# Kernel optimization log

Hardware: AMD Instinct MI355X
Metric: run time of the kernel (lower is better)

Reference implementation:

```python
import jax, jax.numpy as jnp
import numpy as np

EPS = 1e-6

def _rms(x, w):
    # RMSNorm over last dim with learned scale w
    var = jnp.mean(x * x, axis=-1, keepdims=True)
    return x * jax.lax.rsqrt(var + EPS) * w

def _split_heads(x, h):
    b, l, hd = x.shape
    return x.reshape(b, l, h, hd // h).transpose(0, 2, 1, 3)  # b h l d

def setup_inputs() -> dict:
    key = jax.random.key(0)
    ks = jax.random.split(key, 12)
    D = 2048          # hidden_size == ip_hidden_states_dim
    H = 16            # n_heads
    Dh = 128          # head_dim
    T = 1280          # timesteps_emb_dim
    B, L, Lip = 2, 2048, 512
    s = 0.02
    return {
        "ip_hidden_states": jax.random.normal(ks[0], (B, Lip, D), jnp.float32),
        "img_query": jax.random.normal(ks[1], (B, L, D), jnp.float32),
        "img_key": jax.random.normal(ks[2], (B, L, D), jnp.float32),
        "img_value": jax.random.normal(ks[3], (B, L, D), jnp.float32),
        "t_emb": jax.random.normal(ks[4], (B, T), jnp.float32),
        "W_ada": jax.random.normal(ks[5], (2 * D, T), jnp.float32) * s,
        "b_ada": jax.random.normal(ks[6], (2 * D,), jnp.float32) * s,
        "W_k_ip": jax.random.normal(ks[7], (D, D), jnp.float32) * s,
        "W_v_ip": jax.random.normal(ks[8], (D, D), jnp.float32) * s,
        "w_q": jnp.ones((Dh,), jnp.float32),
        "w_k": jnp.ones((Dh,), jnp.float32),
        "w_ipk": jnp.ones((Dh,), jnp.float32),
        "n_heads": H,
    }

def reference(ip_hidden_states, img_query, img_key, img_value, t_emb,
              W_ada, b_ada, W_k_ip, W_v_ip, w_q, w_k, w_ipk, n_heads):
    D = img_query.shape[-1]
    # AdaLayerNorm (mode='normal'): silu -> linear -> shift/scale, LN(no affine)
    emb = jax.nn.silu(t_emb) @ W_ada.T + b_ada          # [B, 2D]
    shift, scale = emb[:, :D], emb[:, D:]
    x = ip_hidden_states
    mu = jnp.mean(x, axis=-1, keepdims=True)
    var = jnp.mean((x - mu) ** 2, axis=-1, keepdims=True)
    xn = (x - mu) * jax.lax.rsqrt(var + 1e-6)
    ip_n = xn * (1.0 + scale[:, None, :]) + shift[:, None, :]
    # K/V projections for IP tokens
    ip_key = ip_n @ W_k_ip.T
    ip_value = ip_n @ W_v_ip.T
    # split heads
    q = _split_heads(img_query, n_heads)   # b h L d
    k = _split_heads(img_key, n_heads)
    v = _split_heads(img_value, n_heads)
    kip = _split_heads(ip_key, n_heads)    # b h Lip d
    vip = _split_heads(ip_value, n_heads)
    # RMSNorms
    q = _rms(q, w_q)
    k = _rms(k, w_k)
    kip = _rms(kip, w_ipk)
    # concat image + IP along sequence
    kcat = jnp.concatenate([k, kip], axis=2)
    vcat = jnp.concatenate([v, vip], axis=2)
    # SDPA
    d = q.shape[-1]
    scores = jnp.einsum('bhld,bhmd->bhlm', q, kcat) / jnp.sqrt(jnp.asarray(d, q.dtype))
    attn = jax.nn.softmax(scores, axis=-1)
    out = jnp.einsum('bhlm,bhmd->bhld', attn, vcat)
    b, h, l, dh = out.shape
    return out.transpose(0, 2, 1, 3).reshape(b, l, h * dh)
```

## Files before the change

kernel.cpp:

```cpp
#include <hip/hip_runtime.h>
#include <hip/hip_bf16.h>

typedef __attribute__((ext_vector_type(8))) __bf16 bf16x8;
typedef __attribute__((ext_vector_type(2))) __bf16 bf16x2;
typedef __attribute__((ext_vector_type(4))) float floatx4;
typedef __attribute__((ext_vector_type(2))) unsigned int uint2v;

#define DEV static __device__ __forceinline__

typedef __attribute__((address_space(1))) const unsigned int gu32;
typedef __attribute__((address_space(3))) unsigned int lu32;

DEV void dma16(const void* g, void* l) {
  __builtin_amdgcn_global_load_lds((gu32*)g, (lu32*)l, 16, 0, 0);
}

DEV unsigned short f2bf(float f) {
  unsigned int u = __float_as_uint(f);
  u += 0x7fffu + ((u >> 16) & 1u);
  return (unsigned short)(u >> 16);
}

DEV unsigned int pk_bf16(float a, float b) {
#if __has_builtin(__builtin_amdgcn_cvt_pk_bf16_f32)
  bf16x2 r = __builtin_amdgcn_cvt_pk_bf16_f32(a, b);
  union { bf16x2 v; unsigned int u; } c; c.v = r;
  return c.u;
#else
  return (unsigned int)f2bf(a) | ((unsigned int)f2bf(b) << 16);
#endif
}

DEV float wred_sum(float v) {
#pragma unroll
  for (int o = 32; o > 0; o >>= 1) v += __shfl_xor(v, o, 64);
  return v;
}

DEV floatx4 mfma32(bf16x8 a, bf16x8 b, floatx4 c) {
  return __builtin_amdgcn_mfma_f32_16x16x32_bf16(a, b, c, 0, 0, 0);
}

#if __has_builtin(__builtin_amdgcn_permlane32_swap) && __has_builtin(__builtin_amdgcn_permlane16_swap)
#define HAS_PLSWAP 1
DEV void p32sw(unsigned int& a, unsigned int& b) {
  uint2v r = __builtin_amdgcn_permlane32_swap(a, b, false, false);
  a = r[0]; b = r[1];
}
DEV void p16sw(unsigned int& a, unsigned int& b) {
  uint2v r = __builtin_amdgcn_permlane16_swap(a, b, false, false);
  a = r[0]; b = r[1];
}
#endif

__global__ void ada_kernel(const float* __restrict__ t_emb, const float* __restrict__ W_ada,
                           const float* __restrict__ b_ada, float* __restrict__ emb) {
  int w = threadIdx.x >> 6, lane = threadIdx.x & 63;
  int gid = blockIdx.x * 4 + w;
  int b = gid >> 12, n = gid & 4095;
  const float* te = t_emb + (size_t)b * 1280;
  const float* wr = W_ada + (size_t)n * 1280;
  float acc = 0.f;
#pragma unroll
  for (int i = 0; i < 20; ++i) {
    int t = lane + i * 64;
    float x = te[t];
    float s = x / (1.f + __expf(-x));
    acc += s * wr[t];
  }
  acc = wred_sum(acc);
  if (lane == 0) emb[gid] = acc + b_ada[n];
}

__global__ void ln_mod_kernel(const float* __restrict__ ip, const float* __restrict__ emb,
                              unsigned short* __restrict__ ipn) {
  int row = blockIdx.x;
  int b = row >> 9;
  int tid = threadIdx.x;
  const float* x = ip + (size_t)row * 2048;
  float xv[8];
  float s1 = 0.f, s2 = 0.f;
  {
    float4 x0 = *(const float4*)&x[tid * 8];
    float4 x1 = *(const float4*)&x[tid * 8 + 4];
    xv[0] = x0.x; xv[1] = x0.y; xv[2] = x0.z; xv[3] = x0.w;
    xv[4] = x1.x; xv[5] = x1.y; xv[6] = x1.z; xv[7] = x1.w;
#pragma unroll
    for (int i = 0; i < 8; ++i) { s1 += xv[i]; s2 += xv[i] * xv[i]; }
  }
  s1 = wred_sum(s1); s2 = wred_sum(s2);
  __shared__ float r1[4], r2[4];
  int w = tid >> 6, lane = tid & 63;
  if (lane == 0) { r1[w] = s1; r2[w] = s2; }
  __syncthreads();
  s1 = r1[0] + r1[1] + r1[2] + r1[3];
  s2 = r2[0] + r2[1] + r2[2] + r2[3];
  float mu = s1 * (1.f / 2048.f);
  float var = s2 * (1.f / 2048.f) - mu * mu;
  float rs = rsqrtf(var + 1e-6f);
  const float* sh = emb + (size_t)b * 4096;
  unsigned short* y = ipn + (size_t)row * 2048;
  unsigned short ob[8];
#pragma unroll
  for (int i = 0; i < 8; ++i) {
    int d = tid * 8 + i;
    float v = (xv[i] - mu) * rs;
    v = v * (1.f + sh[2048 + d]) + sh[d];
    ob[i] = f2bf(v);
  }
  int dst = (tid & ~7) | ((tid & 7) ^ (row & 7));
  *(uint4*)&y[dst * 8] = *(const uint4*)ob;
}

__global__ void cvtw_kernel(const float* __restrict__ wk, const float* __restrict__ wv,
                            unsigned short* __restrict__ wk16, unsigned short* __restrict__ wv16) {
  int row = blockIdx.x, tid = threadIdx.x;
  size_t gi = (size_t)row * 2048 + tid * 8;
  int dst = (tid & ~7) | ((tid & 7) ^ (row & 7));
  size_t o = (size_t)row * 2048 + (size_t)dst * 8;
  float4 a0 = *(const float4*)(wk + gi), a1 = *(const float4*)(wk + gi + 4);
  float4 b0 = *(const float4*)(wv + gi), b1 = *(const float4*)(wv + gi + 4);
  unsigned short oa[8] = { f2bf(a0.x), f2bf(a0.y), f2bf(a0.z), f2bf(a0.w),
                           f2bf(a1.x), f2bf(a1.y), f2bf(a1.z), f2bf(a1.w) };
  unsigned short ob[8] = { f2bf(b0.x), f2bf(b0.y), f2bf(b0.z), f2bf(b0.w),
                           f2bf(b1.x), f2bf(b1.y), f2bf(b1.z), f2bf(b1.w) };
  *(uint4*)(wk16 + o) = *(const uint4*)oa;
  *(uint4*)(wv16 + o) = *(const uint4*)ob;
}

__global__ __launch_bounds__(256) void proj_gemm(const unsigned short* __restrict__ A,
    const unsigned short* __restrict__ Wk, const unsigned short* __restrict__ Wv,
    float* __restrict__ Ck, float* __restrict__ Cv) {
  const unsigned short* Bm = blockIdx.z ? Wv : Wk;
  float* C = blockIdx.z ? Cv : Ck;
  int n0 = blockIdx.x * 64, m0 = blockIdx.y * 128;
  __shared__ __align__(16) unsigned char smem[49152];
  int tid = threadIdx.x, w = tid >> 6, lane = tid & 63, quad = lane >> 4, l16 = lane & 15;
  int xr = l16 & 7;
  floatx4 acc[2][4];
#pragma unroll
  for (int i = 0; i < 2; ++i)
#pragma unroll
    for (int j = 0; j < 4; ++j) { floatx4 z = {0.f, 0.f, 0.f, 0.f}; acc[i][j] = z; }

  const char* Abase = (const char*)A + (size_t)m0 * 4096;
  const char* Bbase = (const char*)Bm + (size_t)n0 * 4096;
  auto stage = [&](int buf, int kk) {
    char* As = (char*)(smem + buf * 24576);
    char* Bs = (char*)(smem + buf * 24576 + 16384);
#pragma unroll
    for (int j = 0; j < 4; ++j) {
      int idx = (w * 4 + j) * 64 + lane;
      dma16(Abase + (size_t)(idx >> 3) * 4096 + kk * 2 + (idx & 7) * 16,
            As + (w * 4 + j) * 1024);
    }
#pragma unroll
    for (int j = 0; j < 2; ++j) {
      int idx = (w * 2 + j) * 64 + lane;
      dma16(Bbase + (size_t)(idx >> 3) * 4096 + kk * 2 + (idx & 7) * 16,
            Bs + (w * 2 + j) * 1024);
    }
  };

  stage(0, 0);
  __syncthreads();
  for (int t = 0; t < 32; ++t) {
    int cur = t & 1;
    if (t < 31) stage(cur ^ 1, (t + 1) * 64);
    const unsigned short* As = (const unsigned short*)(smem + cur * 24576);
    const unsigned short* Bs = (const unsigned short*)(smem + cur * 24576 + 16384);
#pragma unroll
    for (int cc = 0; cc < 2; ++cc) {
      int pc = ((quad + 4 * cc) ^ xr) * 8;
      bf16x8 a0 = *(const bf16x8*)&As[(w * 32 + l16) * 64 + pc];
      bf16x8 a1 = *(const bf16x8*)&As[(w * 32 + 16 + l16) * 64 + pc];
#pragma unroll
      for (int nt = 0; nt < 4; ++nt) {
        bf16x8 bb = *(const bf16x8*)&Bs[(nt * 16 + l16) * 64 + pc];
        acc[0][nt] = mfma32(a0, bb, acc[0][nt]);
        acc[1][nt] = mfma32(a1, bb, acc[1][nt]);
      }
    }
    __syncthreads();
  }
#pragma unroll
  for (int rt = 0; rt < 2; ++rt)
#pragma unroll
    for (int nt = 0; nt < 4; ++nt)
#pragma unroll
      for (int r = 0; r < 4; ++r)
        C[(size_t)(m0 + w * 32 + rt * 16 + quad * 4 + r) * 2048 + n0 + nt * 16 + l16] = acc[rt][nt][r];
}

struct us4 { unsigned short a, b, c, d; };
__global__ __launch_bounds__(256) void kv_build(const float* __restrict__ img_key, const float* __restrict__ img_value,
                         const float* __restrict__ ipk, const float* __restrict__ ipv,
                         const float* __restrict__ w_k, const float* __restrict__ w_ipk,
                         unsigned short* __restrict__ Kc, unsigned short* __restrict__ VtT) {
  int bh = blockIdx.x;
  int mt = blockIdx.y;
  int b = bh >> 4, hh = bh & 15;
  int m0 = mt * 64;
  __shared__ __align__(16) unsigned short Vs[64 * 132];
  int tid = threadIdx.x;
  int mrow = tid >> 2, dq = tid & 3;
  int m = m0 + mrow;
  size_t base;
  const float* wsrc;
  const float *ksrc, *vsrc;
  if (m < 2048) {
    base = (size_t)(b * 2048 + m) * 2048 + hh * 128;
    ksrc = img_key + base; vsrc = img_value + base; wsrc = w_k;
  } else {
    base = (size_t)(b * 512 + (m - 2048)) * 2048 + hh * 128;
    ksrc = ipk + base; vsrc = ipv + base; wsrc = w_ipk;
  }
  float kvv[32]; float ss = 0.f;
  const float4* k4 = (const float4*)ksrc;
#pragma unroll
  for (int i = 0; i < 8; ++i) {
    float4 x = k4[dq * 8 + i];
    kvv[i * 4 + 0] = x.x; kvv[i * 4 + 1] = x.y; kvv[i * 4 + 2] = x.z; kvv[i * 4 + 3] = x.w;
    ss += x.x * x.x + x.y * x.y + x.z * x.z + x.w * x.w;
  }
  ss += __shfl_xor(ss, 1, 64);
  ss += __shfl_xor(ss, 2, 64);
  float rs = rsqrtf(ss * (1.f / 128.f) + 1e-6f);
  unsigned short kb[32];
#pragma unroll
  for (int j = 0; j < 32; ++j) kb[j] = f2bf(kvv[j] * rs * wsrc[dq * 32 + j]);
  uint4* kdst = (uint4*)&Kc[((size_t)bh * 2560 + m) * 128];
#pragma unroll
  for (int i = 0; i < 4; ++i) kdst[(dq * 4 + i) ^ (m & 7)] = ((const uint4*)kb)[i];
  const float4* v4 = (const float4*)vsrc;
#pragma unroll
  for (int i = 0; i < 8; ++i) {
    float4 x = v4[dq * 8 + i];
    us4 p = { f2bf(x.x), f2bf(x.y), f2bf(x.z), f2bf(x.w) };
    *(us4*)&Vs[mrow * 132 + dq * 32 + i * 4] = p;
  }
  __syncthreads();
  int d = tid >> 1, half = tid & 1;
  unsigned short ob[32];
#pragma unroll
  for (int j = 0; j < 32; ++j) ob[j] = Vs[(half * 32 + j) * 132 + d];
  uint4* vdst = (uint4*)&VtT[((size_t)(bh * 40 + mt)) * 8192 + d * 64];
#pragma unroll
  for (int i = 0; i < 4; ++i) vdst[(half * 4 + i) ^ (d & 7)] = ((const uint4*)ob)[i];
}

__global__ __launch_bounds__(256, 2) void attn_kernel(const float* __restrict__ Qf,
    const float* __restrict__ w_q,
    const unsigned short* __restrict__ Kc, const unsigned short* __restrict__ VtT,
    float* __restrict__ out) {
  const float SCL = 0.12751744f;
  const float FM = 17.0f;
  int n = blockIdx.x;
  int xcd = n & 7, jj = n >> 3;
  int bh = xcd * 4 + (jj >> 4);
  int qt2 = jj & 15;
  int b = bh >> 4, hh = bh & 15;
  int tid = threadIdx.x, w = tid >> 6, lane = tid & 63, quad = lane >> 4, l16 = lane & 15;
  int xr = l16 & 7;

  __shared__ __align__(16) unsigned char smem[65536];

  int q0 = qt2 * 128;

  bf16x8 aq[2][4];
#pragma unroll
  for (int qtl = 0; qtl < 2; ++qtl) {
    int qrow = q0 + w * 32 + qtl * 16 + l16;
    const float* src = Qf + ((size_t)(b * 2048 + qrow)) * 2048 + hh * 128;
    float xs[32]; float ss = 0.f;
#pragma unroll
    for (int c = 0; c < 4; ++c) {
      float4 a = *(const float4*)&src[quad * 8 + c * 32];
      float4 b2 = *(const float4*)&src[quad * 8 + c * 32 + 4];
      xs[c * 8 + 0] = a.x;  xs[c * 8 + 1] = a.y;  xs[c * 8 + 2] = a.z;  xs[c * 8 + 3] = a.w;
      xs[c * 8 + 4] = b2.x; xs[c * 8 + 5] = b2.y; xs[c * 8 + 6] = b2.z; xs[c * 8 + 7] = b2.w;
      ss += a.x * a.x + a.y * a.y + a.z * a.z + a.w * a.w
          + b2.x * b2.x + b2.y * b2.y + b2.z * b2.z + b2.w * b2.w;
    }
    ss += __shfl_xor(ss, 16, 64);
    ss += __shfl_xor(ss, 32, 64);
    float rs = rsqrtf(ss * (1.f / 128.f) + 1e-6f);
#pragma unroll
    for (int c = 0; c < 4; ++c) {
      float4 wa = *(const float4*)&w_q[quad * 8 + c * 32];
      float4 wb = *(const float4*)&w_q[quad * 8 + c * 32 + 4];
      union { unsigned int u[4]; bf16x8 v; } pk;
      pk.u[0] = pk_bf16(xs[c * 8 + 0] * rs * wa.x, xs[c * 8 + 1] * rs * wa.y);
      pk.u[1] = pk_bf16(xs[c * 8 + 2] * rs * wa.z, xs[c * 8 + 3] * rs * wa.w);
      pk.u[2] = pk_bf16(xs[c * 8 + 4] * rs * wb.x, xs[c * 8 + 5] * rs * wb.y);
      pk.u[3] = pk_bf16(xs[c * 8 + 6] * rs * wb.z, xs[c * 8 + 7] * rs * wb.w);
      aq[qtl][c] = pk.v;
    }
  }

  const unsigned short* Kb = Kc + (size_t)bh * 2560 * 128;
  const unsigned short* Vb = VtT + (size_t)bh * 40 * 8192;

  floatx4 acc[2][8];
#pragma unroll
  for (int i = 0; i < 2; ++i)
#pragma unroll
    for (int j = 0; j < 8; ++j) { floatx4 z = {0.f, 0.f, 0.f, 0.f}; acc[i][j] = z; }
  float rsum[2] = {0.f, 0.f};

  int seg = w * 4;
  auto stage = [&](int buf, int t) {
    const unsigned short* Ksrc = Kb + (size_t)t * 8192;
    const unsigned short* Vsrc = Vb + (size_t)t * 8192;
    unsigned short* Kt = (unsigned short*)(smem + buf * 32768);
    unsigned short* Vd = (unsigned short*)(smem + buf * 32768 + 16384);
#pragma unroll
    for (int j = 0; j < 4; ++j) {
      int off = (seg + j) * 512 + lane * 8;
      dma16(Ksrc + off, Kt + (seg + j) * 512);
      dma16(Vsrc + off, Vd + (seg + j) * 512);
    }
  };

  stage(0, 0);
  __syncthreads();

  for (int t = 0; t < 40; ++t) {
    int cur = t & 1;
    if (t < 39) stage(cur ^ 1, t + 1);
    const unsigned short* Kt = (const unsigned short*)(smem + cur * 32768);
    const unsigned short* Vs = (const unsigned short*)(smem + cur * 32768 + 16384);

    floatx4 sacc[4][2];
#pragma unroll
    for (int ms = 0; ms < 4; ++ms)
#pragma unroll
      for (int j = 0; j < 2; ++j) { floatx4 z = {0.f, 0.f, 0.f, 0.f}; sacc[ms][j] = z; }
#pragma unroll
    for (int ms = 0; ms < 4; ++ms) {
      int krow = (ms * 16 + l16) * 128;
#pragma unroll
      for (int c = 0; c < 4; ++c) {
        bf16x8 bk = *(const bf16x8*)&Kt[krow + ((quad + c * 4) ^ xr) * 8];
        sacc[ms][0] = mfma32(bk, aq[0][c], sacc[ms][0]);
        sacc[ms][1] = mfma32(bk, aq[1][c], sacc[ms][1]);
      }
    }

    union { unsigned int u[4]; bf16x8 v; } pf[2][2];
#pragma unroll
    for (int mc = 0; mc < 2; ++mc) {
#pragma unroll
      for (int qtl = 0; qtl < 2; ++qtl) {
        float pA[4], pB[4];
#pragma unroll
        for (int r = 0; r < 4; ++r) {
          pA[r] = __builtin_amdgcn_exp2f(fmaf(sacc[mc * 2][qtl][r], SCL, -FM));
          pB[r] = __builtin_amdgcn_exp2f(fmaf(sacc[mc * 2 + 1][qtl][r], SCL, -FM));
        }
        rsum[qtl] += (pA[0] + pA[1]) + (pA[2] + pA[3])
                   + (pB[0] + pB[1]) + (pB[2] + pB[3]);
        unsigned int R0 = pk_bf16(pA[0], pA[1]);
        unsigned int R1 = pk_bf16(pA[2], pA[3]);
        unsigned int R2 = pk_bf16(pB[0], pB[1]);
        unsigned int R3 = pk_bf16(pB[2], pB[3]);
#ifdef HAS_PLSWAP
        p32sw(R0, R2);
        p32sw(R1, R3);
        p16sw(R0, R2);
        p16sw(R1, R3);
        pf[mc][qtl].u[0] = R0; pf[mc][qtl].u[1] = R1;
        pf[mc][qtl].u[2] = R2; pf[mc][qtl].u[3] = R3;
#else
        int base = ((quad & 1) * 2) * 16 + l16;
        int base2 = base + 16;
        unsigned int a0 = __shfl((int)R0, base, 64),  b0 = __shfl((int)R2, base, 64);
        unsigned int a1 = __shfl((int)R1, base, 64),  b1 = __shfl((int)R3, base, 64);
        unsigned int a2 = __shfl((int)R0, base2, 64), b2 = __shfl((int)R2, base2, 64);
        unsigned int a3 = __shfl((int)R1, base2, 64), b3 = __shfl((int)R3, base2, 64);
        bool hi = (quad >> 1) != 0;
        pf[mc][qtl].u[0] = hi ? b0 : a0;
        pf[mc][qtl].u[1] = hi ? b1 : a1;
        pf[mc][qtl].u[2] = hi ? b2 : a2;
        pf[mc][qtl].u[3] = hi ? b3 : a3;
#endif
      }
    }

#pragma unroll
    for (int dt = 0; dt < 8; ++dt) {
      int vrow = (dt * 16 + l16) * 64;
#pragma unroll
      for (int mc = 0; mc < 2; ++mc) {
        bf16x8 va = *(const bf16x8*)&Vs[vrow + ((mc * 4 + quad) ^ xr) * 8];
        acc[0][dt] = mfma32(va, pf[mc][0].v, acc[0][dt]);
        acc[1][dt] = mfma32(va, pf[mc][1].v, acc[1][dt]);
      }
    }
    __syncthreads();
  }

  rsum[0] += __shfl_xor(rsum[0], 16, 64); rsum[0] += __shfl_xor(rsum[0], 32, 64);
  rsum[1] += __shfl_xor(rsum[1], 16, 64); rsum[1] += __shfl_xor(rsum[1], 32, 64);
#pragma unroll
  for (int qtl = 0; qtl < 2; ++qtl) {
    float inv = 1.f / rsum[qtl];
    int qrow = q0 + w * 32 + qtl * 16 + l16;
    float* orow = out + ((size_t)(b * 2048 + qrow)) * 2048 + hh * 128;
#pragma unroll
    for (int dt = 0; dt < 8; ++dt) {
      floatx4 r = acc[qtl][dt] * inv;
      *(floatx4*)&orow[dt * 16 + quad * 4] = r;
    }
  }
}

extern "C" void kernel_launch(void* const* d_in, const int* in_sizes, int n_in,
                              void* d_out, int out_size, void* d_ws, size_t ws_size,
                              hipStream_t stream) {
  const float* ip    = (const float*)d_in[0];
  const float* q     = (const float*)d_in[1];
  const float* k     = (const float*)d_in[2];
  const float* v     = (const float*)d_in[3];
  const float* temb  = (const float*)d_in[4];
  const float* wada  = (const float*)d_in[5];
  const float* bada  = (const float*)d_in[6];
  const float* wkip  = (const float*)d_in[7];
  const float* wvip  = (const float*)d_in[8];
  const float* w_q   = (const float*)d_in[9];
  const float* w_k   = (const float*)d_in[10];
  const float* w_ipk = (const float*)d_in[11];
  float* out = (float*)d_out;
  char* ws = (char*)d_ws;

  float* emb           = (float*)(ws + 0);
  unsigned short* ipn  = (unsigned short*)(ws + 32768);
  unsigned short* wk16 = (unsigned short*)(ws + 4227072);
  unsigned short* wv16 = (unsigned short*)(ws + 12615680);
  unsigned short* Kcat = (unsigned short*)(ws + 16777216);
  unsigned short* VtT  = (unsigned short*)(ws + 37748736);
  float* ipk           = (float*)(ws + 58720256);
  float* ipv           = (float*)(ws + 67108864);

  ada_kernel<<<dim3(2048), dim3(256), 0, stream>>>(temb, wada, bada, emb);
  ln_mod_kernel<<<dim3(1024), dim3(256), 0, stream>>>(ip, emb, ipn);
  cvtw_kernel<<<dim3(2048), dim3(256), 0, stream>>>(wkip, wvip, wk16, wv16);
  proj_gemm<<<dim3(32, 8, 2), dim3(256), 0, stream>>>(ipn, wk16, wv16, ipk, ipv);
  kv_build<<<dim3(32, 40), dim3(256), 0, stream>>>(k, v, ipk, ipv, w_k, w_ipk, Kcat, VtT);
  attn_kernel<<<dim3(512), dim3(256), 0, stream>>>(q, w_q, Kcat, VtT, out);
}
```

Baseline: 330.6 us.

## Triple-buffer projection GEMM with vmcnt waits and merge LN/weight-convert kernels

The projection GEMM moves from double to triple-buffered LDS staging. It prefetches two K-tiles ahead and waits with explicit s_waitcnt vmcnt counts plus raw s_barrier instead of __syncthreads, so more global-to-LDS DMA is in flight while MFMAs run. Separately, the LayerNorm-modulate and weight bf16 conversion kernels are merged into one launch, branching on block index, to save a kernel launch. The GEMM's LDS use grows from 48KB to 72KB per block, which may lower occupancy, and the hand-written vmcnt counts must match the number of DMAs issued per stage.

```diff
diff --git a/kernel.cpp b/kernel.cpp
--- a/kernel.cpp
+++ b/kernel.cpp
@@ -72,60 +72,62 @@
   if (lane == 0) emb[gid] = acc + b_ada[n];
 }
 
-__global__ void ln_mod_kernel(const float* __restrict__ ip, const float* __restrict__ emb,
-                              unsigned short* __restrict__ ipn) {
-  int row = blockIdx.x;
-  int b = row >> 9;
+__global__ void lncvt_kernel(const float* __restrict__ ip, const float* __restrict__ emb,
+                             unsigned short* __restrict__ ipn,
+                             const float* __restrict__ wk, const float* __restrict__ wv,
+                             unsigned short* __restrict__ wk16, unsigned short* __restrict__ wv16) {
+  int blk = blockIdx.x;
   int tid = threadIdx.x;
-  const float* x = ip + (size_t)row * 2048;
-  float xv[8];
-  float s1 = 0.f, s2 = 0.f;
-  {
-    float4 x0 = *(const float4*)&x[tid * 8];
-    float4 x1 = *(const float4*)&x[tid * 8 + 4];
-    xv[0] = x0.x; xv[1] = x0.y; xv[2] = x0.z; xv[3] = x0.w;
-    xv[4] = x1.x; xv[5] = x1.y; xv[6] = x1.z; xv[7] = x1.w;
-#pragma unroll
-    for (int i = 0; i < 8; ++i) { s1 += xv[i]; s2 += xv[i] * xv[i]; }
-  }
-  s1 = wred_sum(s1); s2 = wred_sum(s2);
-  __shared__ float r1[4], r2[4];
-  int w = tid >> 6, lane = tid & 63;
-  if (lane == 0) { r1[w] = s1; r2[w] = s2; }
-  __syncthreads();
-  s1 = r1[0] + r1[1] + r1[2] + r1[3];
-  s2 = r2[0] + r2[1] + r2[2] + r2[3];
-  float mu = s1 * (1.f / 2048.f);
-  float var = s2 * (1.f / 2048.f) - mu * mu;
-  float rs = rsqrtf(var + 1e-6f);
-  const float* sh = emb + (size_t)b * 4096;
-  unsigned short* y = ipn + (size_t)row * 2048;
-  unsigned short ob[8];
-#pragma unroll
-  for (int i = 0; i < 8; ++i) {
-    int d = tid * 8 + i;
-    float v = (xv[i] - mu) * rs;
-    v = v * (1.f + sh[2048 + d]) + sh[d];
-    ob[i] = f2bf(v);
-  }
-  int dst = (tid & ~7) | ((tid & 7) ^ (row & 7));
-  *(uint4*)&y[dst * 8] = *(const uint4*)ob;
-}
-
-__global__ void cvtw_kernel(const float* __restrict__ wk, const float* __restrict__ wv,
-                            unsigned short* __restrict__ wk16, unsigned short* __restrict__ wv16) {
-  int row = blockIdx.x, tid = threadIdx.x;
-  size_t gi = (size_t)row * 2048 + tid * 8;
-  int dst = (tid & ~7) | ((tid & 7) ^ (row & 7));
-  size_t o = (size_t)row * 2048 + (size_t)dst * 8;
-  float4 a0 = *(const float4*)(wk + gi), a1 = *(const float4*)(wk + gi + 4);
-  float4 b0 = *(const float4*)(wv + gi), b1 = *(const float4*)(wv + gi + 4);
-  unsigned short oa[8] = { f2bf(a0.x), f2bf(a0.y), f2bf(a0.z), f2bf(a0.w),
-                           f2bf(a1.x), f2bf(a1.y), f2bf(a1.z), f2bf(a1.w) };
-  unsigned short ob[8] = { f2bf(b0.x), f2bf(b0.y), f2bf(b0.z), f2bf(b0.w),
-                           f2bf(b1.x), f2bf(b1.y), f2bf(b1.z), f2bf(b1.w) };
-  *(uint4*)(wk16 + o) = *(const uint4*)oa;
-  *(uint4*)(wv16 + o) = *(const uint4*)ob;
+  if (blk < 1024) {
+    int row = blk;
+    int b = row >> 9;
+    const float* x = ip + (size_t)row * 2048;
+    float xv[8];
+    float s1 = 0.f, s2 = 0.f;
+    {
+      float4 x0 = *(const float4*)&x[tid * 8];
+      float4 x1 = *(const float4*)&x[tid * 8 + 4];
+      xv[0] = x0.x; xv[1] = x0.y; xv[2] = x0.z; xv[3] = x0.w;
+      xv[4] = x1.x; xv[5] = x1.y; xv[6] = x1.z; xv[7] = x1.w;
+#pragma unroll
+      for (int i = 0; i < 8; ++i) { s1 += xv[i]; s2 += xv[i] * xv[i]; }
+    }
+    s1 = wred_sum(s1); s2 = wred_sum(s2);
+    __shared__ float r1[4], r2[4];
+    int w = tid >> 6, lane = tid & 63;
+    if (lane == 0) { r1[w] = s1; r2[w] = s2; }
+    __syncthreads();
+    s1 = r1[0] + r1[1] + r1[2] + r1[3];
+    s2 = r2[0] + r2[1] + r2[2] + r2[3];
+    float mu = s1 * (1.f / 2048.f);
+    float var = s2 * (1.f / 2048.f) - mu * mu;
+    float rs = rsqrtf(var + 1e-6f);
+    const float* sh = emb + (size_t)b * 4096;
+    unsigned short* y = ipn + (size_t)row * 2048;
+    unsigned short ob[8];
+#pragma unroll
+    for (int i = 0; i < 8; ++i) {
+      int d = tid * 8 + i;
+      float v = (xv[i] - mu) * rs;
+      v = v * (1.f + sh[2048 + d]) + sh[d];
+      ob[i] = f2bf(v);
+    }
+    int dst = (tid & ~7) | ((tid & 7) ^ (row & 7));
+    *(uint4*)&y[dst * 8] = *(const uint4*)ob;
+  } else {
+    int row = blk - 1024;
+    size_t gi = (size_t)row * 2048 + tid * 8;
+    int dst = (tid & ~7) | ((tid & 7) ^ (row & 7));
+    size_t o = (size_t)row * 2048 + (size_t)dst * 8;
+    float4 a0 = *(const float4*)(wk + gi), a1 = *(const float4*)(wk + gi + 4);
+    float4 b0 = *(const float4*)(wv + gi), b1 = *(const float4*)(wv + gi + 4);
+    unsigned short oa[8] = { f2bf(a0.x), f2bf(a0.y), f2bf(a0.z), f2bf(a0.w),
+                             f2bf(a1.x), f2bf(a1.y), f2bf(a1.z), f2bf(a1.w) };
+    unsigned short ob2[8] = { f2bf(b0.x), f2bf(b0.y), f2bf(b0.z), f2bf(b0.w),
+                              f2bf(b1.x), f2bf(b1.y), f2bf(b1.z), f2bf(b1.w) };
+    *(uint4*)(wk16 + o) = *(const uint4*)oa;
+    *(uint4*)(wv16 + o) = *(const uint4*)ob2;
+  }
 }
 
 __global__ __launch_bounds__(256) void proj_gemm(const unsigned short* __restrict__ A,
@@ -134,7 +136,7 @@
   const unsigned short* Bm = blockIdx.z ? Wv : Wk;
   float* C = blockIdx.z ? Cv : Ck;
   int n0 = blockIdx.x * 64, m0 = blockIdx.y * 128;
-  __shared__ __align__(16) unsigned char smem[49152];
+  __shared__ __align__(16) unsigned char smem[73728];
   int tid = threadIdx.x, w = tid >> 6, lane = tid & 63, quad = lane >> 4, l16 = lane & 15;
   int xr = l16 & 7;
   floatx4 acc[2][4];
@@ -163,10 +165,16 @@
   };
 
   stage(0, 0);
-  __syncthreads();
+  stage(1, 64);
+  int cur = 0;
   for (int t = 0; t < 32; ++t) {
-    int cur = t & 1;
-    if (t < 31) stage(cur ^ 1, (t + 1) * 64);
+    int pre = cur + 2; if (pre >= 3) pre -= 3;
+    if (t + 2 < 32) stage(pre, (t + 2) * 64);
+    if (t < 30)       asm volatile("s_waitcnt vmcnt(12)" ::: "memory");
+    else if (t == 30) asm volatile("s_waitcnt vmcnt(6)" ::: "memory");
+    else              asm volatile("s_waitcnt vmcnt(0)" ::: "memory");
+    __builtin_amdgcn_sched_barrier(0);
+    __builtin_amdgcn_s_barrier();
     const unsigned short* As = (const unsigned short*)(smem + cur * 24576);
     const unsigned short* Bs = (const unsigned short*)(smem + cur * 24576 + 16384);
 #pragma unroll
@@ -181,7 +189,8 @@
         acc[1][nt] = mfma32(a1, bb, acc[1][nt]);
       }
     }
-    __syncthreads();
+    __builtin_amdgcn_s_barrier();
+    cur = cur + 1; if (cur >= 3) cur = 0;
   }
 #pragma unroll
   for (int rt = 0; rt < 2; ++rt)
@@ -443,8 +452,7 @@
   float* ipv           = (float*)(ws + 67108864);
 
   ada_kernel<<<dim3(2048), dim3(256), 0, stream>>>(temb, wada, bada, emb);
-  ln_mod_kernel<<<dim3(1024), dim3(256), 0, stream>>>(ip, emb, ipn);
-  cvtw_kernel<<<dim3(2048), dim3(256), 0, stream>>>(wkip, wvip, wk16, wv16);
+  lncvt_kernel<<<dim3(3072), dim3(256), 0, stream>>>(ip, emb, ipn, wkip, wvip, wk16, wv16);
   proj_gemm<<<dim3(32, 8, 2), dim3(256), 0, stream>>>(ipn, wk16, wv16, ipk, ipv);
   kv_build<<<dim3(32, 40), dim3(256), 0, stream>>>(k, v, ipk, ipv, w_k, w_ipk, Kcat, VtT);
   attn_kernel<<<dim3(512), dim3(256), 0, stream>>>(q, w_q, Kcat, VtT, out);
```

After: 333.5 us. About the same (+0.9%).
